# Optimization experiments

Measured on AMD Instinct MI355X. Metric: run time of the kernel, lower is better.

The kernel has to match this reference:

```python
import jax, jax.numpy as jnp
import numpy as np


def _conv1x1(x, w):
    # x [N,I,D,H,W], w [O,I]
    return jnp.einsum('nidhw,oi->nodhw', x, w)


def _conv3x3(x, w):
    return jax.lax.conv_general_dilated(
        x, w, window_strides=(1, 1, 1), padding=[(1, 1)] * 3,
        dimension_numbers=('NCDHW', 'OIDHW', 'NCDHW'))


def _interp_axis(x, out_len, axis):
    # linear interpolation along one axis, align_corners=True
    in_len = x.shape[axis]
    scale = (in_len - 1) / (out_len - 1)
    pos = jnp.arange(out_len, dtype=x.dtype) * scale
    lo = jnp.clip(jnp.floor(pos).astype(jnp.int32), 0, in_len - 1)
    hi = jnp.minimum(lo + 1, in_len - 1)
    frac = pos - lo.astype(x.dtype)
    shp = [1] * x.ndim
    shp[axis] = out_len
    frac = frac.reshape(shp)
    return jnp.take(x, lo, axis=axis) * (1 - frac) + jnp.take(x, hi, axis=axis) * frac


def _upsample_trilinear_ac(x, size):
    for ax, s in zip((2, 3, 4), size):
        x = _interp_axis(x, s, ax)
    return x


def _grid_sample_3d(inp, grid):
    # inp [N,C,D,H,W]; grid [N,Do,Ho,Wo,3] with channels (x=w, y=h, z=d) in [-1,1]
    # matches torch grid_sample defaults: trilinear, align_corners=False, zeros padding
    N, C, D, H, W = inp.shape
    ix = ((grid[..., 0] + 1) * W - 1) * 0.5
    iy = ((grid[..., 1] + 1) * H - 1) * 0.5
    iz = ((grid[..., 2] + 1) * D - 1) * 0.5
    x0 = jnp.floor(ix).astype(jnp.int32)
    y0 = jnp.floor(iy).astype(jnp.int32)
    z0 = jnp.floor(iz).astype(jnp.int32)
    fx = ix - x0.astype(inp.dtype)
    fy = iy - y0.astype(inp.dtype)
    fz = iz - z0.astype(inp.dtype)
    flat = inp.reshape(N, C, D * H * W)
    out = jnp.zeros((N, C) + grid.shape[1:4], dtype=inp.dtype)
    for dz, wz in ((0, 1 - fz), (1, fz)):
        for dy, wy in ((0, 1 - fy), (1, fy)):
            for dx, wx in ((0, 1 - fx), (1, fx)):
                zc = z0 + dz
                yc = y0 + dy
                xc = x0 + dx
                valid = (zc >= 0) & (zc < D) & (yc >= 0) & (yc < H) & (xc >= 0) & (xc < W)
                idx = (jnp.clip(zc, 0, D - 1) * H + jnp.clip(yc, 0, H - 1)) * W + jnp.clip(xc, 0, W - 1)
                vals = jax.vmap(lambda f, i: f[:, i])(flat, idx)  # [N,C,Do,Ho,Wo]
                w = (wz * wy * wx) * valid.astype(inp.dtype)
                out = out + vals * w[:, None]
    return out


def _point_reinforce(x, w_atten, w_conv):
    # SE-style: global avg pool -> 1x1 conv -> sigmoid -> residual scale -> 1x1 conv
    pooled = jnp.mean(x, axis=(2, 3, 4), keepdims=True)
    atten = jax.nn.sigmoid(_conv1x1(pooled, w_atten))
    x = x + x * atten
    return _conv1x1(x, w_conv)


def _forward(x, y, w_down_h, w_down_l, w_flow, w_att_atten, w_att_conv):
    D, H, W = x.shape[2:]
    low = _conv1x1(x, w_down_l)
    low = _point_reinforce(low, w_att_atten, w_att_conv)
    hf = _conv1x1(y, w_down_h)
    hf = _upsample_trilinear_ac(hf, (D, H, W))
    flow = _conv3x3(jnp.concatenate([hf, low], axis=1), w_flow)  # [N,3,D,H,W]
    # coordinate grid, channel order (w, h, d) as in the original flow_warp
    gw = jnp.broadcast_to(jnp.arange(W, dtype=x.dtype)[None, None, :], (D, H, W))
    gh = jnp.broadcast_to(jnp.arange(H, dtype=x.dtype)[None, :, None], (D, H, W))
    gd = jnp.broadcast_to(jnp.arange(D, dtype=x.dtype)[:, None, None], (D, H, W))
    grid = jnp.stack([gw, gh, gd], axis=0)[None]  # [1,3,D,H,W]
    norm = jnp.array([W, H, D], dtype=x.dtype)
    # NOTE: faithful to original -- divides by size only (grid ends up in [0,1), not [-1,1])
    vgrid = jnp.transpose(grid + flow, (0, 2, 3, 4, 1)) / norm  # [N,D,H,W,3]
    return _grid_sample_3d(y, vgrid)


def setup_inputs() -> dict:
    key = jax.random.key(0)
    ks = jax.random.split(key, 7)
    inplane_l, inplane_h, outplane = 64, 128, 64
    x = jax.random.normal(ks[0], (2, inplane_l, 16, 64, 64), dtype=jnp.float32)
    y = jax.random.normal(ks[1], (2, inplane_h, 8, 32, 32), dtype=jnp.float32)
    s = 0.05
    w_down_h = jax.random.normal(ks[2], (outplane, inplane_h), dtype=jnp.float32) * s
    w_down_l = jax.random.normal(ks[3], (outplane, inplane_l), dtype=jnp.float32) * s
    w_flow = jax.random.normal(ks[4], (3, 2 * outplane, 3, 3, 3), dtype=jnp.float32) * s
    w_att_atten = jax.random.normal(ks[5], (inplane_l, inplane_l), dtype=jnp.float32) * s
    w_att_conv = jax.random.normal(ks[6], (inplane_l, inplane_l), dtype=jnp.float32) * s
    return {'x': x, 'y': y, 'w_down_h': w_down_h, 'w_down_l': w_down_l,
            'w_flow': w_flow, 'w_att_atten': w_att_atten, 'w_att_conv': w_att_conv}


def reference(x, y, w_down_h, w_down_l, w_flow, w_att_atten, w_att_conv):
    return _forward(x, y, w_down_h, w_down_l, w_flow, w_att_atten, w_att_conv)
```

## Files before the change

kernel.cpp:

```cpp
#include <hip/hip_runtime.h>
#include <math.h>


#define MEANX_OFF  0
#define WCOMBT_OFF 128
#define HF_OFF     8320
#define LOW2_OFF   1056896
#define HFUP_OFF   9445504
#define VG_OFF     17834112
#define ZPAGE_OFF  18227328

__global__ __launch_bounds__(256) void kearly(const float* __restrict__ x,
                                              const float* __restrict__ y,
                                              const float* __restrict__ wdh,
                                              float* __restrict__ meanx,
                                              float* __restrict__ hf,
                                              float* __restrict__ zpage) {
    const int blk = blockIdx.x;
    if (blk < 128) {
        if (blk == 0 && threadIdx.x < 64) zpage[threadIdx.x] = 0.f;
        int ch = blk;
        const float4* base = (const float4*)(x + (size_t)ch * 65536);
        float s = 0.f;
        for (int j = threadIdx.x; j < 16384; j += 256) {
            float4 v = base[j];
            s += v.x + v.y + v.z + v.w;
        }
        __shared__ float red[256];
        red[threadIdx.x] = s;
        __syncthreads();
        for (int off = 128; off > 0; off >>= 1) {
            if (threadIdx.x < off) red[threadIdx.x] += red[threadIdx.x + off];
            __syncthreads();
        }
        if (threadIdx.x == 0) meanx[ch] = red[0] * (1.0f / 65536.0f);
    } else {
        const int b = blk - 128;
        const int n = b >> 7;
        const int r = b & 127;
        const int os = r & 3;
        const int tile = r >> 2;
        const int p = tile * 256 + threadIdx.x;
        const float* yb = y + (size_t)n * 128 * 8192 + p;

        float acc[16];
#pragma unroll
        for (int o = 0; o < 16; ++o) acc[o] = 0.f;

        for (int i = 0; i < 128; i += 4) {
            const float yi0 = yb[(size_t)(i + 0) * 8192];
            const float yi1 = yb[(size_t)(i + 1) * 8192];
            const float yi2 = yb[(size_t)(i + 2) * 8192];
            const float yi3 = yb[(size_t)(i + 3) * 8192];
#pragma unroll
            for (int o = 0; o < 16; ++o) {
                float a = acc[o];
                a = fmaf(wdh[(os * 16 + o) * 128 + i + 0], yi0, a);
                a = fmaf(wdh[(os * 16 + o) * 128 + i + 1], yi1, a);
                a = fmaf(wdh[(os * 16 + o) * 128 + i + 2], yi2, a);
                a = fmaf(wdh[(os * 16 + o) * 128 + i + 3], yi3, a);
                acc[o] = a;
            }
        }
        float* ob = hf + (size_t)(n * 64 + os * 16) * 8192 + p;
#pragma unroll
        for (int o = 0; o < 16; ++o)
            ob[(size_t)o * 8192] = acc[o];
    }
}

__global__ __launch_bounds__(256) void kprep(const float* __restrict__ wdl,
                                             const float* __restrict__ watt,
                                             const float* __restrict__ wconv,
                                             const float* __restrict__ meanx,
                                             float* __restrict__ wcombT) {
    const int n = blockIdx.x;
    const int tid = threadIdx.x;
    __shared__ float s_wdl[4096];
    __shared__ float s_wcT[4096];
    __shared__ float pooled[64], sc[64];
    for (int k = tid; k < 4096; k += 256) {
        s_wdl[k] = wdl[k];
        int o = k >> 6, j = k & 63;
        s_wcT[j * 64 + o] = wconv[k];
    }
    __syncthreads();
    if (tid < 64) {
        float p = 0.f;
        for (int i = 0; i < 64; ++i) p += s_wdl[tid * 64 + i] * meanx[n * 64 + i];
        pooled[tid] = p;
    }
    __syncthreads();
    if (tid < 64) {
        float a = 0.f;
        for (int i = 0; i < 64; ++i) a += watt[tid * 64 + i] * pooled[i];
        sc[tid] = 1.f + 1.f / (1.f + expf(-a));
    }
    __syncthreads();
    for (int k = 0; k < 16; ++k) {
        const int idx = tid + 256 * k;
        const int o = idx & 63, i = idx >> 6;
        float acc = 0.f;
#pragma unroll 8
        for (int j = 0; j < 64; ++j)
            acc += s_wcT[j * 64 + o] * (sc[j] * s_wdl[j * 64 + i]);
        wcombT[n * 4096 + i * 64 + o] = acc;
    }
}

__global__ __launch_bounds__(256) void kmid(const float* __restrict__ x,
                                            const float* __restrict__ wcombT,
                                            const float* __restrict__ hf,
                                            float* __restrict__ low2,
                                            float* __restrict__ hfup) {
    const int blk = blockIdx.x;
    if (blk < 512) {
        const int b = blk;
        const int n = b >> 8;
        const int r = b & 255;
        const int os = r & 1;
        const int tile = r >> 1;
        const int p = tile * 512 + 2 * threadIdx.x;
        const float* xb = x + (size_t)n * 64 * 65536 + p;
        const float* wr = wcombT + n * 4096 + os * 32;

        float2 acc[32];
#pragma unroll
        for (int o = 0; o < 32; ++o) acc[o] = make_float2(0.f, 0.f);

        for (int i = 0; i < 64; i += 2) {
            const float2 xi0 = *(const float2*)(xb + (size_t)(i + 0) * 65536);
            const float2 xi1 = *(const float2*)(xb + (size_t)(i + 1) * 65536);
#pragma unroll
            for (int o = 0; o < 32; ++o) {
                const float w0 = wr[(i + 0) * 64 + o];
                const float w1 = wr[(i + 1) * 64 + o];
                acc[o].x = fmaf(w0, xi0.x, acc[o].x);
                acc[o].y = fmaf(w0, xi0.y, acc[o].y);
                acc[o].x = fmaf(w1, xi1.x, acc[o].x);
                acc[o].y = fmaf(w1, xi1.y, acc[o].y);
            }
        }
        float* ob = low2 + (size_t)(n * 64 + os * 32) * 65536 + p;
#pragma unroll
        for (int o = 0; o < 32; ++o)
            *(float2*)(ob + (size_t)o * 65536) = acc[o];
    } else {
        int id2 = (blk - 512) * 256 + threadIdx.x;
        int wp = id2 & 31, h = (id2 >> 5) & 63, d = (id2 >> 11) & 15;
        int c = (id2 >> 15) & 63, n = id2 >> 21;
        const float SD = 7.0f / 15.0f, SH = 31.0f / 63.0f;
        float pd = (float)d * SD, ph = (float)h * SH;
        int z0 = (int)pd; if (z0 > 7) z0 = 7;
        int z1 = min(z0 + 1, 7); float fz = pd - (float)z0;
        int y0 = (int)ph; if (y0 > 31) y0 = 31;
        int y1 = min(y0 + 1, 31); float fy = ph - (float)y0;

        const int w0i = 2 * wp, w1i = 2 * wp + 1;
        float pw0 = (float)w0i * SH, pw1 = (float)w1i * SH;
        int xa = (int)pw0; if (xa > 31) xa = 31;
        float fx0 = pw0 - (float)xa;
        int xb2 = (int)pw1; if (xb2 > 31) xb2 = 31;
        float fx1 = pw1 - (float)xb2;

        const float* b = hf + (size_t)(n * 64 + c) * 8192;
        const int r00 = (z0 * 32 + y0) * 32, r01 = (z0 * 32 + y1) * 32;
        const int r10 = (z1 * 32 + y0) * 32, r11 = (z1 * 32 + y1) * 32;
        const float wzy00 = (1.f - fz) * (1.f - fy), wzy01 = (1.f - fz) * fy;
        const float wzy10 = fz * (1.f - fy), wzy11 = fz * fy;

        float colv[3];
#pragma unroll
        for (int j = 0; j < 3; ++j) {
            int xc = min(xa + j, 31);
            colv[j] = wzy00 * b[r00 + xc] + wzy01 * b[r01 + xc] +
                      wzy10 * b[r10 + xc] + wzy11 * b[r11 + xc];
        }
        float o0 = colv[0] + (colv[1] - colv[0]) * fx0;
        int i1 = xb2 - xa;
        float lo = (i1 == 0) ? colv[0] : colv[1];
        float hi = (i1 == 0) ? colv[1] : colv[2];
        float o1 = lo + (hi - lo) * fx1;

        *(float2*)(hfup + ((size_t)id2 * 2)) = make_float2(o0, o1);
    }
}

__global__ __launch_bounds__(256) void kflowp(const float* __restrict__ ws,
                                              const float* __restrict__ wflow,
                                              float* __restrict__ part) {
    const int tid = threadIdx.x;
    const int b = blockIdx.x;
    const int split = b & 15;
    const int tile = b >> 4;
    const int n = tile >> 6;
    const int t = tile & 63;
    const int td = t >> 4, th = (t >> 2) & 3, tw = t & 3;
    const int d0 = td * 4, h0 = th * 16, w0 = tw * 16;
    const int xo = tid & 3, ty = (tid >> 2) & 15, tz = tid >> 6;
    const int wv = tid >> 6;

    __shared__ float lds[3][2048];

    const int srcb = (split < 8)
        ? HFUP_OFF + (n * 64 + split * 8) * 65536
        : LOW2_OFF + (n * 64 + (split - 8) * 8) * 65536;

    int woff[8];
#pragma unroll
    for (int k = 0; k < 8; ++k) {
        const int e = tid + 256 * k;
        const int r = e / 18;
        const int lx = e - r * 18;
        const int z = r / 18;
        const int ly = r - z * 18;
        const int gz = d0 - 1 + z, gy = h0 - 1 + ly, gx = w0 - 1 + lx;
        const bool ok = (e < 1944) && ((unsigned)gz < 16u) && ((unsigned)gy < 64u) &&
                        ((unsigned)gx < 64u);
        woff[k] = ok ? (srcb + gz * 4096 + gy * 64 + gx) : ZPAGE_OFF;
    }

#define STAGE(BUFI, CI)                                                               \
    {                                                                                 \
        _Pragma("unroll")                                                             \
        for (int k = 0; k < 8; ++k) {                                                 \
            const int off = woff[k] + ((woff[k] < ZPAGE_OFF) ? (CI) * 65536 : 0);     \
            __builtin_amdgcn_global_load_lds(                                         \
                (const __attribute__((address_space(1))) unsigned int*)(ws + off),    \
                (__attribute__((address_space(3))) unsigned int*)                     \
                    (&lds[BUFI][wv * 64 + 256 * k]),                                  \
                4, 0, 0);                                                             \
        }                                                                             \
    }

    float acc[3][4];
#pragma unroll
    for (int o = 0; o < 3; ++o)
#pragma unroll
        for (int j = 0; j < 4; ++j) acc[o][j] = 0.f;

    STAGE(0, 0);

    for (int ci = 0; ci < 8; ++ci) {
        const int cur = ci % 3;
        if (ci < 7) {
            STAGE((ci + 1) % 3, ci + 1);
            asm volatile("s_waitcnt vmcnt(8)" ::: "memory");
        } else {
            asm volatile("s_waitcnt vmcnt(0)" ::: "memory");
        }
        __builtin_amdgcn_s_barrier();
        __builtin_amdgcn_sched_barrier(0);

        const int cgs = __builtin_amdgcn_readfirstlane(split * 8 + ci);
        const float* wb = wflow + (size_t)cgs * 27;
        const float* buf = lds[cur];
#pragma unroll
        for (int dz = 0; dz < 3; ++dz) {
#pragma unroll
            for (int dy = 0; dy < 3; ++dy) {
                const float* rp = &buf[((tz + dz) * 18 + ty + dy) * 18 + 4 * xo];
                const float2 a0 = *(const float2*)(rp);
                const float2 a1 = *(const float2*)(rp + 2);
                const float2 a2 = *(const float2*)(rp + 4);
                const float v[6] = {a0.x, a0.y, a1.x, a1.y, a2.x, a2.y};
                float wq[3][3];
#pragma unroll
                for (int o = 0; o < 3; ++o)
#pragma unroll
                    for (int dx = 0; dx < 3; ++dx)
                        wq[o][dx] = wb[o * 3456 + (dz * 3 + dy) * 3 + dx];
#pragma unroll
                for (int o = 0; o < 3; ++o)
#pragma unroll
                    for (int j = 0; j < 4; ++j)
#pragma unroll
                        for (int dx = 0; dx < 3; ++dx)
                            acc[o][j] = fmaf(wq[o][dx], v[j + dx], acc[o][j]);
            }
        }
    }
#undef STAGE

    const int oz = d0 + tz, oy = h0 + ty, ox = w0 + 4 * xo;
    const size_t base = ((size_t)(split * 2 + n)) * 3 * 65536;
    const int p = oz * 4096 + oy * 64 + ox;
#pragma unroll
    for (int o = 0; o < 3; ++o)
        *(float4*)(part + base + (size_t)o * 65536 + p) =
            make_float4(acc[o][0], acc[o][1], acc[o][2], acc[o][3]);
}

__global__ __launch_bounds__(256) void kpost(const float* __restrict__ part,
                                             const float* __restrict__ y,
                                             float* __restrict__ vg,
                                             float* __restrict__ yt) {
    const int blk = blockIdx.x;
    if (blk < 128) {
        int gid = blk * 256 + threadIdx.x;
        int n = gid >> 14, p4 = (gid & 16383) * 4;
        float4 s0 = make_float4(0.f, 0.f, 0.f, 0.f);
        float4 s1 = s0, s2 = s0;
        for (int s = 0; s < 16; ++s) {
            const float* bp = part + ((size_t)(s * 2 + n)) * 3 * 65536 + p4;
            float4 a = *(const float4*)(bp);
            float4 b4 = *(const float4*)(bp + 65536);
            float4 c4 = *(const float4*)(bp + 131072);
            s0.x += a.x; s0.y += a.y; s0.z += a.z; s0.w += a.w;
            s1.x += b4.x; s1.y += b4.y; s1.z += b4.z; s1.w += b4.w;
            s2.x += c4.x; s2.y += c4.y; s2.z += c4.z; s2.w += c4.w;
        }
        int w = p4 & 63, h = (p4 >> 6) & 63, d = p4 >> 12;
        size_t vb = (size_t)n * 3 * 65536;
        *(float4*)(vg + vb + p4) = make_float4(
            ((float)(w + 0) + s0.x) * (1.0f / 64.0f), ((float)(w + 1) + s0.y) * (1.0f / 64.0f),
            ((float)(w + 2) + s0.z) * (1.0f / 64.0f), ((float)(w + 3) + s0.w) * (1.0f / 64.0f));
        *(float4*)(vg + vb + 65536 + p4) = make_float4(
            ((float)h + s1.x) * (1.0f / 64.0f), ((float)h + s1.y) * (1.0f / 64.0f),
            ((float)h + s1.z) * (1.0f / 64.0f), ((float)h + s1.w) * (1.0f / 64.0f));
        *(float4*)(vg + vb + 131072 + p4) = make_float4(
            ((float)d + s2.x) * (1.0f / 16.0f), ((float)d + s2.y) * (1.0f / 16.0f),
            ((float)d + s2.z) * (1.0f / 16.0f), ((float)d + s2.w) * (1.0f / 16.0f));
    } else {
        int b = blk - 128;
        int n = b >> 8;
        int rem = b & 255;
        int ct = rem >> 7, st = rem & 127;
        int c0 = ct * 64, s0 = st * 64;
        __shared__ float t[64][65];
        int tx = threadIdx.x & 63, ty = threadIdx.x >> 6;
#pragma unroll
        for (int k = 0; k < 16; ++k)
            t[ty + 4 * k][tx] = y[((size_t)(n * 128 + c0 + ty + 4 * k)) * 8192 + s0 + tx];
        __syncthreads();
#pragma unroll
        for (int k = 0; k < 16; ++k)
            yt[((size_t)(n * 8192 + s0 + ty + 4 * k)) * 128 + c0 + tx] = t[tx][ty + 4 * k];
    }
}

__global__ __launch_bounds__(256) void ksample(const float* __restrict__ yt,
                                               const float* __restrict__ vg,
                                               float* __restrict__ out) {
    const int b = blockIdx.x;
    const int n = b >> 10;
    const int p0 = (b & 1023) << 6;
    const int tid = threadIdx.x;
    const int lane = tid & 63;
    const int wv = tid >> 6;

    __shared__ float lds[128 * 65];

    const float* ytn = yt + (size_t)n * 8192 * 128;
    const size_t vb = (size_t)n * 3 * 65536;

    for (int q = 0; q < 16; ++q) {
        const int pt = wv * 16 + q;
        const int p = p0 + pt;
        float gx = vg[vb + p], gy = vg[vb + 65536 + p], gz = vg[vb + 131072 + p];
        float ix = ((gx + 1.f) * 32.f - 1.f) * 0.5f;
        float iy = ((gy + 1.f) * 32.f - 1.f) * 0.5f;
        float iz = ((gz + 1.f) * 8.f - 1.f) * 0.5f;
        int x0 = (int)floorf(ix), y0 = (int)floorf(iy), z0 = (int)floorf(iz);
        float fx = ix - (float)x0, fy = iy - (float)y0, fz = iz - (float)z0;
        float wx[2] = {1.f - fx, fx}, wy[2] = {1.f - fy, fy}, wz[2] = {1.f - fz, fz};
        int idx8[8];
        float w8[8];
        float wsum = 0.f;
#pragma unroll
        for (int k = 0; k < 8; ++k) {
            int dz = k >> 2, dy = (k >> 1) & 1, dx = k & 1;
            int zc = z0 + dz, yc = y0 + dy, xc = x0 + dx;
            bool valid = ((unsigned)zc < 8u) && ((unsigned)yc < 32u) && ((unsigned)xc < 32u);
            int zcl = min(max(zc, 0), 7), ycl = min(max(yc, 0), 31), xcl = min(max(xc, 0), 31);
            idx8[k] = (zcl * 32 + ycl) * 32 + xcl;
            float wgt = wz[dz] * wy[dy] * wx[dx];
            w8[k] = valid ? wgt : 0.f;
            wsum += w8[k];
        }
        float ax = 0.f, ay = 0.f;
        if (wsum != 0.f) {
#pragma unroll
            for (int k = 0; k < 8; ++k) {
                const float2 v = *(const float2*)(ytn + (size_t)idx8[k] * 128 + 2 * lane);
                ax = fmaf(w8[k], v.x, ax);
                ay = fmaf(w8[k], v.y, ay);
            }
        }
        lds[(2 * lane) * 65 + pt] = ax;
        lds[(2 * lane + 1) * 65 + pt] = ay;
    }
    __syncthreads();
    const int pw = tid & 63, cw = tid >> 6;
    float* ob = out + (size_t)n * 128 * 65536 + p0 + pw;
#pragma unroll
    for (int k = 0; k < 32; ++k) {
        int c = k * 4 + cw;
        ob[(size_t)c * 65536] = lds[c * 65 + pw];
    }
}

extern "C" void kernel_launch(void* const* d_in, const int* in_sizes, int n_in,
                              void* d_out, int out_size, void* d_ws, size_t ws_size,
                              hipStream_t stream) {
    const float* x     = (const float*)d_in[0];
    const float* y     = (const float*)d_in[1];
    const float* wdh   = (const float*)d_in[2];
    const float* wdl   = (const float*)d_in[3];
    const float* wflow = (const float*)d_in[4];
    const float* watt  = (const float*)d_in[5];
    const float* wconv = (const float*)d_in[6];
    float* out = (float*)d_out;

    float* ws     = (float*)d_ws;
    float* meanx  = ws + MEANX_OFF;
    float* wcombT = ws + WCOMBT_OFF;
    float* hf     = ws + HF_OFF;
    float* low2   = ws + LOW2_OFF;
    float* hfup   = ws + HFUP_OFF;
    float* vg     = ws + VG_OFF;
    float* zpage  = ws + ZPAGE_OFF;

    float* part = out;
    float* yt = hfup;

    kearly<<<384, 256, 0, stream>>>(x, y, wdh, meanx, hf, zpage);
    kprep<<<2, 256, 0, stream>>>(wdl, watt, wconv, meanx, wcombT);
    kmid<<<16896, 256, 0, stream>>>(x, wcombT, hf, low2, hfup);
    kflowp<<<2048, 256, 0, stream>>>(ws, wflow, part);
    kpost<<<640, 256, 0, stream>>>(part, y, vg, yt);
    ksample<<<2048, 256, 0, stream>>>(yt, vg, out);
}
```

Baseline: 173.5 us.

## Fold low-path 1x1 channel mix into flow conv weights, drop low2 buffer

Premultiplies the per-batch combined 1x1 weight matrix into the second half of the 3x3x3 flow convolution weights in kprep. kflowp then convolves the raw x input directly, so the low2 intermediate no longer has to be computed and stored. This removes a 64x64 pointwise GEMM over the full 16x64x64 volume, plus a 32 MB write and read. In exchange kprep does extra serial work on only two blocks, and kflowp uses per-batch weights with a different stride.

```diff
diff --git a/kernel.cpp b/kernel.cpp
--- a/kernel.cpp
+++ b/kernel.cpp
@@ -3,12 +3,11 @@
 
 
 #define MEANX_OFF  0
-#define WCOMBT_OFF 128
-#define HF_OFF     8320
-#define LOW2_OFF   1056896
-#define HFUP_OFF   9445504
-#define VG_OFF     17834112
-#define ZPAGE_OFF  18227328
+#define WEFF_OFF   128
+#define HF_OFF     16384
+#define HFUP_OFF   1064960
+#define VG_OFF     9453568
+#define ZPAGE_OFF  9846784
 
 __global__ __launch_bounds__(256) void kearly(const float* __restrict__ x,
                                               const float* __restrict__ y,
@@ -72,18 +71,24 @@
 __global__ __launch_bounds__(256) void kprep(const float* __restrict__ wdl,
                                              const float* __restrict__ watt,
                                              const float* __restrict__ wconv,
+                                             const float* __restrict__ wflow,
                                              const float* __restrict__ meanx,
-                                             float* __restrict__ wcombT) {
+                                             float* __restrict__ weff) {
     const int n = blockIdx.x;
     const int tid = threadIdx.x;
     __shared__ float s_wdl[4096];
     __shared__ float s_wcT[4096];
+    __shared__ float s_flow[5184];
     __shared__ float pooled[64], sc[64];
     for (int k = tid; k < 4096; k += 256) {
         s_wdl[k] = wdl[k];
         int o = k >> 6, j = k & 63;
         s_wcT[j * 64 + o] = wconv[k];
     }
+    for (int k = tid; k < 5184; k += 256) {
+        int o = k / 1728, r = k - o * 1728;
+        s_flow[k] = wflow[o * 3456 + 1728 + r];
+    }
     __syncthreads();
     if (tid < 64) {
         float p = 0.f;
@@ -97,6 +102,8 @@
         sc[tid] = 1.f + 1.f / (1.f + expf(-a));
     }
     __syncthreads();
+    float wc[16];
+#pragma unroll
     for (int k = 0; k < 16; ++k) {
         const int idx = tid + 256 * k;
         const int o = idx & 63, i = idx >> 6;
@@ -104,90 +111,72 @@
 #pragma unroll 8
         for (int j = 0; j < 64; ++j)
             acc += s_wcT[j * 64 + o] * (sc[j] * s_wdl[j * 64 + i]);
-        wcombT[n * 4096 + i * 64 + o] = acc;
-    }
-}
-
-__global__ __launch_bounds__(256) void kmid(const float* __restrict__ x,
-                                            const float* __restrict__ wcombT,
-                                            const float* __restrict__ hf,
-                                            float* __restrict__ low2,
+        wc[k] = acc;
+    }
+    __syncthreads();
+#pragma unroll
+    for (int k = 0; k < 16; ++k) {
+        const int idx = tid + 256 * k;
+        const int o = idx & 63, i = idx >> 6;
+        s_wdl[i * 64 + o] = wc[k];
+    }
+    __syncthreads();
+    for (int e = tid; e < 5184; e += 256) {
+        const int i = e / 81, r = e - i * 81;
+        const int o = r / 27, tap = r - o * 27;
+        float acc = 0.f;
+#pragma unroll 8
+        for (int c = 0; c < 64; ++c)
+            acc += s_flow[o * 1728 + c * 27 + tap] * s_wdl[i * 64 + c];
+        weff[n * 5184 + e] = acc;
+    }
+}
+
+__global__ __launch_bounds__(256) void kmid(const float* __restrict__ hf,
                                             float* __restrict__ hfup) {
-    const int blk = blockIdx.x;
-    if (blk < 512) {
-        const int b = blk;
-        const int n = b >> 8;
-        const int r = b & 255;
-        const int os = r & 1;
-        const int tile = r >> 1;
-        const int p = tile * 512 + 2 * threadIdx.x;
-        const float* xb = x + (size_t)n * 64 * 65536 + p;
-        const float* wr = wcombT + n * 4096 + os * 32;
-
-        float2 acc[32];
-#pragma unroll
-        for (int o = 0; o < 32; ++o) acc[o] = make_float2(0.f, 0.f);
-
-        for (int i = 0; i < 64; i += 2) {
-            const float2 xi0 = *(const float2*)(xb + (size_t)(i + 0) * 65536);
-            const float2 xi1 = *(const float2*)(xb + (size_t)(i + 1) * 65536);
-#pragma unroll
-            for (int o = 0; o < 32; ++o) {
-                const float w0 = wr[(i + 0) * 64 + o];
-                const float w1 = wr[(i + 1) * 64 + o];
-                acc[o].x = fmaf(w0, xi0.x, acc[o].x);
-                acc[o].y = fmaf(w0, xi0.y, acc[o].y);
-                acc[o].x = fmaf(w1, xi1.x, acc[o].x);
-                acc[o].y = fmaf(w1, xi1.y, acc[o].y);
-            }
-        }
-        float* ob = low2 + (size_t)(n * 64 + os * 32) * 65536 + p;
-#pragma unroll
-        for (int o = 0; o < 32; ++o)
-            *(float2*)(ob + (size_t)o * 65536) = acc[o];
-    } else {
-        int id2 = (blk - 512) * 256 + threadIdx.x;
-        int wp = id2 & 31, h = (id2 >> 5) & 63, d = (id2 >> 11) & 15;
-        int c = (id2 >> 15) & 63, n = id2 >> 21;
-        const float SD = 7.0f / 15.0f, SH = 31.0f / 63.0f;
-        float pd = (float)d * SD, ph = (float)h * SH;
-        int z0 = (int)pd; if (z0 > 7) z0 = 7;
-        int z1 = min(z0 + 1, 7); float fz = pd - (float)z0;
-        int y0 = (int)ph; if (y0 > 31) y0 = 31;
-        int y1 = min(y0 + 1, 31); float fy = ph - (float)y0;
-
-        const int w0i = 2 * wp, w1i = 2 * wp + 1;
-        float pw0 = (float)w0i * SH, pw1 = (float)w1i * SH;
-        int xa = (int)pw0; if (xa > 31) xa = 31;
-        float fx0 = pw0 - (float)xa;
-        int xb2 = (int)pw1; if (xb2 > 31) xb2 = 31;
-        float fx1 = pw1 - (float)xb2;
-
-        const float* b = hf + (size_t)(n * 64 + c) * 8192;
-        const int r00 = (z0 * 32 + y0) * 32, r01 = (z0 * 32 + y1) * 32;
-        const int r10 = (z1 * 32 + y0) * 32, r11 = (z1 * 32 + y1) * 32;
-        const float wzy00 = (1.f - fz) * (1.f - fy), wzy01 = (1.f - fz) * fy;
-        const float wzy10 = fz * (1.f - fy), wzy11 = fz * fy;
-
-        float colv[3];
-#pragma unroll
-        for (int j = 0; j < 3; ++j) {
-            int xc = min(xa + j, 31);
-            colv[j] = wzy00 * b[r00 + xc] + wzy01 * b[r01 + xc] +
-                      wzy10 * b[r10 + xc] + wzy11 * b[r11 + xc];
-        }
-        float o0 = colv[0] + (colv[1] - colv[0]) * fx0;
-        int i1 = xb2 - xa;
-        float lo = (i1 == 0) ? colv[0] : colv[1];
-        float hi = (i1 == 0) ? colv[1] : colv[2];
-        float o1 = lo + (hi - lo) * fx1;
-
-        *(float2*)(hfup + ((size_t)id2 * 2)) = make_float2(o0, o1);
-    }
+    int id2 = blockIdx.x * 256 + threadIdx.x;
+    int wp = id2 & 31, h = (id2 >> 5) & 63, d = (id2 >> 11) & 15;
+    int c = (id2 >> 15) & 63, n = id2 >> 21;
+    const float SD = 7.0f / 15.0f, SH = 31.0f / 63.0f;
+    float pd = (float)d * SD, ph = (float)h * SH;
+    int z0 = (int)pd; if (z0 > 7) z0 = 7;
+    int z1 = min(z0 + 1, 7); float fz = pd - (float)z0;
+    int y0 = (int)ph; if (y0 > 31) y0 = 31;
+    int y1 = min(y0 + 1, 31); float fy = ph - (float)y0;
+
+    const int w0i = 2 * wp, w1i = 2 * wp + 1;
+    float pw0 = (float)w0i * SH, pw1 = (float)w1i * SH;
+    int xa = (int)pw0; if (xa > 31) xa = 31;
+    float fx0 = pw0 - (float)xa;
+    int xb2 = (int)pw1; if (xb2 > 31) xb2 = 31;
+    float fx1 = pw1 - (float)xb2;
+
+    const float* b = hf + (size_t)(n * 64 + c) * 8192;
+    const int r00 = (z0 * 32 + y0) * 32, r01 = (z0 * 32 + y1) * 32;
+    const int r10 = (z1 * 32 + y0) * 32, r11 = (z1 * 32 + y1) * 32;
+    const float wzy00 = (1.f - fz) * (1.f - fy), wzy01 = (1.f - fz) * fy;
+    const float wzy10 = fz * (1.f - fy), wzy11 = fz * fy;
+
+    float colv[3];
+#pragma unroll
+    for (int j = 0; j < 3; ++j) {
+        int xc = min(xa + j, 31);
+        colv[j] = wzy00 * b[r00 + xc] + wzy01 * b[r01 + xc] +
+                  wzy10 * b[r10 + xc] + wzy11 * b[r11 + xc];
+    }
+    float o0 = colv[0] + (colv[1] - colv[0]) * fx0;
+    int i1 = xb2 - xa;
+    float lo = (i1 == 0) ? colv[0] : colv[1];
+    float hi = (i1 == 0) ? colv[1] : colv[2];
+    float o1 = lo + (hi - lo) * fx1;
+
+    *(float2*)(hfup + ((size_t)id2 * 2)) = make_float2(o0, o1);
 }
 
 __global__ __launch_bounds__(256) void kflowp(const float* __restrict__ ws,
+                                              const float* __restrict__ x,
                                               const float* __restrict__ wflow,
+                                              const float* __restrict__ weff,
                                               float* __restrict__ part) {
     const int tid = threadIdx.x;
     const int b = blockIdx.x;
@@ -202,11 +191,13 @@
 
     __shared__ float lds[3][2048];
 
-    const int srcb = (split < 8)
-        ? HFUP_OFF + (n * 64 + split * 8) * 65536
-        : LOW2_OFF + (n * 64 + (split - 8) * 8) * 65536;
-
-    int woff[8];
+    const float* gb = (split < 8)
+        ? ws + HFUP_OFF + (size_t)(n * 64 + split * 8) * 65536
+        : x + (size_t)(n * 64 + (split - 8) * 8) * 65536;
+    const float* zp = ws + ZPAGE_OFF;
+
+    const float* addrk[8];
+    int strk[8];
 #pragma unroll
     for (int k = 0; k < 8; ++k) {
         const int e = tid + 256 * k;
@@ -217,16 +208,17 @@
         const int gz = d0 - 1 + z, gy = h0 - 1 + ly, gx = w0 - 1 + lx;
         const bool ok = (e < 1944) && ((unsigned)gz < 16u) && ((unsigned)gy < 64u) &&
                         ((unsigned)gx < 64u);
-        woff[k] = ok ? (srcb + gz * 4096 + gy * 64 + gx) : ZPAGE_OFF;
+        addrk[k] = ok ? (gb + (gz * 4096 + gy * 64 + gx)) : zp;
+        strk[k] = ok ? 65536 : 0;
     }
 
 #define STAGE(BUFI, CI)                                                               \
     {                                                                                 \
         _Pragma("unroll")                                                             \
         for (int k = 0; k < 8; ++k) {                                                 \
-            const int off = woff[k] + ((woff[k] < ZPAGE_OFF) ? (CI) * 65536 : 0);     \
             __builtin_amdgcn_global_load_lds(                                         \
-                (const __attribute__((address_space(1))) unsigned int*)(ws + off),    \
+                (const __attribute__((address_space(1))) unsigned int*)               \
+                    (addrk[k] + (size_t)(CI) * strk[k]),                              \
                 (__attribute__((address_space(3))) unsigned int*)                     \
                     (&lds[BUFI][wv * 64 + 256 * k]),                                  \
                 4, 0, 0);                                                             \
@@ -252,8 +244,12 @@
         __builtin_amdgcn_s_barrier();
         __builtin_amdgcn_sched_barrier(0);
 
-        const int cgs = __builtin_amdgcn_readfirstlane(split * 8 + ci);
-        const float* wb = wflow + (size_t)cgs * 27;
+        const int cidx = __builtin_amdgcn_readfirstlane(
+            (split < 8) ? (split * 8 + ci) : ((split - 8) * 8 + ci));
+        const float* wbase;
+        int wos;
+        if (split < 8) { wbase = wflow + (size_t)cidx * 27; wos = 3456; }
+        else           { wbase = weff + (size_t)n * 5184 + (size_t)cidx * 81; wos = 27; }
         const float* buf = lds[cur];
 #pragma unroll
         for (int dz = 0; dz < 3; ++dz) {
@@ -269,7 +265,7 @@
                 for (int o = 0; o < 3; ++o)
 #pragma unroll
                     for (int dx = 0; dx < 3; ++dx)
-                        wq[o][dx] = wb[o * 3456 + (dz * 3 + dy) * 3 + dx];
+                        wq[o][dx] = wbase[o * wos + (dz * 3 + dy) * 3 + dx];
 #pragma unroll
                 for (int o = 0; o < 3; ++o)
 #pragma unroll
@@ -414,9 +410,8 @@
 
     float* ws     = (float*)d_ws;
     float* meanx  = ws + MEANX_OFF;
-    float* wcombT = ws + WCOMBT_OFF;
+    float* weff   = ws + WEFF_OFF;
     float* hf     = ws + HF_OFF;
-    float* low2   = ws + LOW2_OFF;
     float* hfup   = ws + HFUP_OFF;
     float* vg     = ws + VG_OFF;
     float* zpage  = ws + ZPAGE_OFF;
@@ -425,9 +420,9 @@
     float* yt = hfup;
 
     kearly<<<384, 256, 0, stream>>>(x, y, wdh, meanx, hf, zpage);
-    kprep<<<2, 256, 0, stream>>>(wdl, watt, wconv, meanx, wcombT);
-    kmid<<<16896, 256, 0, stream>>>(x, wcombT, hf, low2, hfup);
-    kflowp<<<2048, 256, 0, stream>>>(ws, wflow, part);
+    kprep<<<2, 256, 0, stream>>>(wdl, watt, wconv, wflow, meanx, weff);
+    kmid<<<16384, 256, 0, stream>>>(hf, hfup);
+    kflowp<<<2048, 256, 0, stream>>>(ws, x, wflow, weff, part);
     kpost<<<640, 256, 0, stream>>>(part, y, vg, yt);
     ksample<<<2048, 256, 0, stream>>>(yt, vg, out);
 }
```

Result: slower. 178.4 us (+2.8%).
